# Performance work log

Hardware: AMD Instinct MI355X
Metric: run time of the kernel (lower is better)

## Reference

```python
import jax, jax.numpy as jnp
import numpy as np
from jax import lax

NUM_HEADS = 8
FACTOR = 2
DIM = 64


def _get_idx(h, w):
    # Frequency-magnitude reordering map from Attention.get_idx_map (static shapes).
    l2 = np.arange(w)[None, :]
    mu = np.arange(h // 2)[:, None] * l2                 # upper half outer product
    md = np.arange(h - h // 2)[::-1][:, None] * l2        # lower half, flipped rows
    m = np.concatenate([mu, md], 0).reshape(-1)
    idx = np.argsort(m, kind='stable')                    # gather permutation
    inv = np.argsort(idx)                                 # scatter (inverse) permutation
    return jnp.asarray(idx), jnp.asarray(inv)


def _dwconv3x3(x, w):
    # depthwise 3x3, stride 1, padding 1 (groups = channels)
    c = x.shape[1]
    return lax.conv_general_dilated(x, w[:, None, :, :], (1, 1), 'SAME',
                                    dimension_numbers=('NCHW', 'OIHW', 'NCHW'),
                                    feature_group_count=c)


def _fft_reorder(t, idx):
    # pad last dim to even, rfft2 (ortho), stack real/imag on channels, gather by idx
    b, c, h, w = t.shape
    pad_w = (-w) % 2
    t = jnp.pad(t, ((0, 0), (0, 0), (0, 0), (0, pad_w)))
    f = jnp.fft.rfft2(t, norm='ortho')                     # [b,c,h,w']
    r = jnp.concatenate([f.real, f.imag], axis=1)          # [b,2c,h,w']
    r = r.reshape(b, 2 * c, -1)[:, :, idx]                 # gather reorder
    return r, pad_w


def _softmax1(x):
    # non-standard softmax: exp(x) / (sum(exp(x)) + 1), no max-subtraction (faithful)
    e = jnp.exp(x)
    return e / (jnp.sum(e, axis=-1, keepdims=True) + 1.0)


def _l2norm(x):
    n = jnp.sqrt(jnp.sum(x * x, axis=-1, keepdims=True))
    return x / jnp.maximum(n, 1e-12)


def _split_heads(t):
    # 'b (head c) (factor hw) -> b head (c factor) hw'
    B, C2, Np = t.shape
    cc = C2 // NUM_HEADS
    t = t.reshape(B, NUM_HEADS, cc, FACTOR, Np // FACTOR)
    return t.reshape(B, NUM_HEADS, cc * FACTOR, Np // FACTOR)


def attention_forward(x, w_qkv, w_dw, w_proj, temperature):
    b, c, h, w = x.shape
    qkv = jnp.einsum('bchw,oc->bohw', x, w_qkv)            # 1x1 conv (3c out)
    qkv = _dwconv3x3(qkv, w_dw)
    q, k, v = jnp.split(qkv, 3, axis=1)

    wprime = (w + ((-w) % 2)) // 2 + 1                     # rfft last-dim size
    idx, inv = _get_idx(h, wprime)

    q, pad_w = _fft_reorder(q, idx)
    k, _ = _fft_reorder(k, idx)
    v, _ = _fft_reorder(v, idx)

    p = (-q.shape[-1]) % FACTOR                            # pad N to multiple of factor
    if p:
        pads = ((0, 0), (0, 0), (0, p))
        q, k, v = jnp.pad(q, pads), jnp.pad(k, pads), jnp.pad(v, pads)

    qh, kh, vh = _split_heads(q), _split_heads(k), _split_heads(v)
    qh, kh = _l2norm(qh), _l2norm(kh)

    attn = jnp.einsum('bhcn,bhdn->bhcd', qh, kh) * temperature[None]  # c x c, per head
    attn = _softmax1(attn)
    o = jnp.einsum('bhcd,bhdn->bhcn', attn, vh)

    # 'b head (c factor) hw -> b (head c) (factor hw)'
    B, H, CF, HW = o.shape
    o = o.reshape(B, H, CF // FACTOR, FACTOR, HW).reshape(B, H * (CF // FACTOR), FACTOR * HW)
    if p:
        o = o[:, :, :o.shape[-1] - p]
    o = o[:, :, inv]                                        # inverse permutation (scatter)
    o = o.reshape(B, 2 * c, h, wprime)
    oc = lax.complex(o[:, :c], o[:, c:])
    o = jnp.fft.irfft2(oc, norm='ortho')                    # [b,c,h,w+pad_w]
    if pad_w:
        o = o[:, :, :, :o.shape[-1] - pad_w]
    return jnp.einsum('bchw,oc->bohw', o, w_proj)           # project_out 1x1 conv


def setup_inputs() -> dict:
    key = jax.random.key(0)
    k1, k2, k3, k4 = jax.random.split(key, 4)
    b, c, h, w = 4, DIM, 256, 256
    return {
        'x': jax.random.normal(k1, (b, c, h, w), dtype=jnp.float32),
        'w_qkv': jax.random.normal(k2, (3 * c, c), dtype=jnp.float32) * 0.05,
        'w_dw': jax.random.normal(k3, (3 * c, 3, 3), dtype=jnp.float32) * 0.05,
        'w_proj': jax.random.normal(k4, (c, c), dtype=jnp.float32) * 0.05,
        'temperature': jnp.ones((NUM_HEADS, 1, 1), dtype=jnp.float32),
    }


def reference(x, w_qkv, w_dw, w_proj, temperature):
    return attention_forward(x, w_qkv, w_dw, w_proj, temperature)
```

## Files before the change

### kernel.cpp

```cpp
#include <hip/hip_runtime.h>
#include <math.h>

#define HW 65536
#define WP 129
#define NPOS 33024
#define NHALF 16512
#define MMAX 16257
#define PI_F 3.14159265358979f

__device__ __forceinline__ int rev7(int x){ return (int)(__brev((unsigned)x) >> 25); }
__device__ __forceinline__ int rev8(int x){ return (int)(__brev((unsigned)x) >> 24); }

__global__ void k_hist(int* __restrict__ hist) {
  int v = blockIdx.x*256 + threadIdx.x;
  if (v >= MMAX) return;
  int cnt;
  if (v == 0) cnt = 512;
  else {
    cnt = 0;
    for (int d = 1; d <= 127; ++d)
      if (v % d == 0 && v / d <= 128) cnt += 2;
  }
  hist[v] = cnt;
}

__global__ void k_scan(const int* __restrict__ hist, int* __restrict__ base) {
  __shared__ int part[512];
  int t = threadIdx.x;
  int lo = t*32, hi = lo+32; if (hi > MMAX) hi = MMAX;
  int s = 0;
  if (lo < MMAX) for (int i = lo; i < hi; ++i) s += hist[i];
  part[t] = s;
  __syncthreads();
  for (int off = 1; off < 512; off <<= 1) {
    int v = (t >= off) ? part[t-off] : 0;
    __syncthreads();
    part[t] += v;
    __syncthreads();
  }
  int acc = part[t] - s;
  if (lo < MMAX) for (int i = lo; i < hi; ++i) { base[i] = acc; acc += hist[i]; }
}

__global__ void k_build(const int* __restrict__ base, int* __restrict__ idx, int* __restrict__ inv) {
  int v = blockIdx.x*256 + threadIdx.x;
  if (v >= MMAX) return;
  int s = base[v];
  if (v == 0) {
    for (int j = 0; j < 129; ++j) { idx[s] = j; inv[j] = s; ++s; }
    for (int i = 1; i < 255; ++i) { int p = i*129; idx[s] = p; inv[p] = s; ++s; }
    for (int j = 0; j < 129; ++j) { int p = 255*129 + j; idx[s] = p; inv[p] = s; ++s; }
  } else {
    for (int i = 1; i < 255; ++i) {
      int d = (i < 128) ? i : 255 - i;
      if (v % d == 0) {
        int j = v / d;
        if (j <= 128) { int p = i*129 + j; idx[s] = p; inv[p] = s; ++s; }
      }
    }
  }
}

__global__ void k_maps(const int* __restrict__ idx, const int* __restrict__ inv,
                       int* __restrict__ partner_t, int* __restrict__ half_t) {
  int t = blockIdx.x*256 + threadIdx.x;
  if (t >= NPOS) return;
  int k = t >> 8, h = t & 255;
  int p = h*129 + k;
  int s = inv[p];
  int f = (s >= NHALF) ? 1 : 0;
  int s2 = f ? (s - NHALF) : (s + NHALF);
  int pp = idx[s2];
  int kk = pp % 129, hh = pp / 129;
  partner_t[t] = kk*256 + hh;
  half_t[t] = f;
}

__global__ void k_maps2(const int* __restrict__ idx,
                        int* __restrict__ t0n, int* __restrict__ t1n) {
  int n = blockIdx.x*256 + threadIdx.x;
  if (n >= NHALF) return;
  int p0 = idx[n], p1 = idx[n + NHALF];
  t0n[n] = (p0 % 129)*256 + p0/129;
  t1n[n] = (p1 % 129)*256 + p1/129;
}

__global__ void k_zero(float* __restrict__ g) {
  int i = blockIdx.x*256 + threadIdx.x;
  if (i < 34816) g[i] = 0.f;
}

__global__ __launch_bounds__(256) void k_conv64(const float* __restrict__ in,
        const float* __restrict__ w, float* __restrict__ outp) {
  __shared__ float wT[64][65];
  __shared__ float xs[16][260];
  int tid = threadIdx.x;
  int ti = tid >> 5, tj = tid & 31;
  int lb = blockIdx.y;
  int px0 = blockIdx.x * 256;
  const float* ib = in + (size_t)lb*64*HW + px0;
  for (int e = tid; e < 4096; e += 256) { int o = e >> 6, c = e & 63; wT[c][o] = w[e]; }
  float acc[64];
  #pragma unroll
  for (int z = 0; z < 64; ++z) acc[z] = 0.f;
  for (int cc = 0; cc < 4; ++cc) {
    __syncthreads();
    for (int e = tid; e < 1024; e += 256) {
      int c = e >> 6, p4 = (e & 63) << 2;
      *(float4*)&xs[c][p4] = *(const float4*)(ib + (size_t)(cc*16 + c)*HW + p4);
    }
    __syncthreads();
    #pragma unroll
    for (int k = 0; k < 16; ++k) {
      float wv[8], xv[8];
      *(float4*)&wv[0] = *(const float4*)&wT[cc*16+k][ti*8];
      *(float4*)&wv[4] = *(const float4*)&wT[cc*16+k][ti*8+4];
      *(float4*)&xv[0] = *(const float4*)&xs[k][tj*8];
      *(float4*)&xv[4] = *(const float4*)&xs[k][tj*8+4];
      #pragma unroll
      for (int o = 0; o < 8; ++o) {
        #pragma unroll
        for (int p = 0; p < 8; ++p)
          acc[o*8+p] += wv[o]*xv[p];
      }
    }
  }
  float* ob = outp + (size_t)lb*64*HW + px0 + tj*8;
  #pragma unroll
  for (int o = 0; o < 8; ++o) {
    *(float4*)(ob + (size_t)(ti*8+o)*HW)     = *(float4*)&acc[o*8];
    *(float4*)(ob + (size_t)(ti*8+o)*HW + 4) = *(float4*)&acc[o*8+4];
  }
}

__global__ __launch_bounds__(512) void k_dwrowfft(const float* __restrict__ tmp,
        const float* __restrict__ wdw, float* __restrict__ planes,
        int tensor, size_t psz) {
  __shared__ float rows[10][260];
  __shared__ float2 Z[8][128];
  __shared__ float2 X[8][132];
  int wave = threadIdx.x >> 6, lane = threadIdx.x & 63;
  int lb = blockIdx.z, c = blockIdx.y;
  int h0 = blockIdx.x * 8;
  const float* ib = tmp + ((size_t)lb*64 + c)*HW;
  for (int e = threadIdx.x; e < 2560; e += 512) {
    int r = e >> 8, col = e & 255;
    int y = h0 - 1 + r;
    rows[r][col] = (y >= 0 && y < 256) ? ib[y*256 + col] : 0.f;
  }
  const float* w9 = wdw + ((size_t)tensor*64 + c)*9;
  float w0=w9[0],w1=w9[1],w2=w9[2],w3=w9[3],w4=w9[4],w5=w9[5],w6=w9[6],w7=w9[7],w8=w9[8];
  __syncthreads();
  float d[4];
  #pragma unroll
  for (int q = 0; q < 4; ++q) {
    int col = (q < 2) ? (2*lane + q) : (128 + 2*lane + (q-2));
    float acc = rows[wave+0][col]*w1 + rows[wave+1][col]*w4 + rows[wave+2][col]*w7;
    if (col > 0)   acc += rows[wave+0][col-1]*w0 + rows[wave+1][col-1]*w3 + rows[wave+2][col-1]*w6;
    if (col < 255) acc += rows[wave+0][col+1]*w2 + rows[wave+1][col+1]*w5 + rows[wave+2][col+1]*w8;
    d[q] = acc;
  }
  Z[wave][rev7(lane)]    = make_float2(d[0], d[1]);
  Z[wave][rev7(lane+64)] = make_float2(d[2], d[3]);
  __syncthreads();
  for (int L = 1; L <= 64; L <<= 1) {
    int kk = lane & (L-1);
    int i0 = ((lane ^ kk) << 1) | kk;
    float sn, cs; sincosf(-PI_F * kk / L, &sn, &cs);
    float2 u = Z[wave][i0], t = Z[wave][i0+L];
    float tr = t.x*cs - t.y*sn;
    float ti = t.x*sn + t.y*cs;
    Z[wave][i0]   = make_float2(u.x+tr, u.y+ti);
    Z[wave][i0+L] = make_float2(u.x-tr, u.y-ti);
    __syncthreads();
  }
  for (int kk = lane; kk <= 128; kk += 64) {
    float2 Zk = Z[wave][kk & 127];
    float2 Zm = Z[wave][(128-kk) & 127];
    float Er = 0.5f*(Zk.x + Zm.x), Ei = 0.5f*(Zk.y - Zm.y);
    float Or = 0.5f*(Zk.y + Zm.y), Oi = 0.5f*(Zm.x - Zk.x);
    float sn, cs; sincosf(-PI_F * kk / 128.0f, &sn, &cs);
    float Xr = Er + cs*Or - sn*Oi;
    float Xi = Ei + cs*Oi + sn*Or;
    X[wave][kk] = make_float2(Xr*(1.0f/256.0f), Xi*(1.0f/256.0f));
  }
  __syncthreads();
  float* pre = planes + (size_t)(tensor*2)*psz + ((size_t)lb*64 + c)*NPOS;
  float* pim = pre + psz;
  for (int e = threadIdx.x; e < 1032; e += 512) {
    int k = e >> 3, hh = e & 7;
    float2 v = X[hh][k];
    pre[(size_t)k*256 + h0 + hh] = v.x;
    pim[(size_t)k*256 + h0 + hh] = v.y;
  }
}

__global__ __launch_bounds__(512) void k_colfft(float* __restrict__ planes,
        int tensor, size_t psz) {
  __shared__ float2 Z[8][258];
  int wave = threadIdx.x >> 6, lane = threadIdx.x & 63;
  int lb = blockIdx.z, c = blockIdx.y;
  int kreal = blockIdx.x*8 + wave;
  int k = (kreal < 129) ? kreal : 128;
  float* pre = planes + (size_t)(tensor*2)*psz + ((size_t)lb*64 + c)*NPOS + (size_t)k*256;
  float* pim = pre + psz;
  #pragma unroll
  for (int i = 0; i < 4; ++i) {
    int h = lane + 64*i;
    Z[wave][rev8(h)] = make_float2(pre[h], pim[h]);
  }
  __syncthreads();
  for (int L = 1; L <= 128; L <<= 1) {
    #pragma unroll
    for (int jj = 0; jj < 2; ++jj) {
      int j = lane + 64*jj;
      int kk = j & (L-1);
      int i0 = ((j ^ kk) << 1) | kk;
      float sn, cs; sincosf(-PI_F * kk / L, &sn, &cs);
      float2 u = Z[wave][i0], t = Z[wave][i0+L];
      float tr = t.x*cs - t.y*sn;
      float ti = t.x*sn + t.y*cs;
      Z[wave][i0]   = make_float2(u.x+tr, u.y+ti);
      Z[wave][i0+L] = make_float2(u.x-tr, u.y-ti);
    }
    __syncthreads();
  }
  if (kreal <= 128) {
    #pragma unroll
    for (int i = 0; i < 4; ++i) {
      float2 v = Z[wave][lane + 64*i];
      pre[lane+64*i] = v.x;
      pim[lane+64*i] = v.y;
    }
  }
}

__global__ __launch_bounds__(256) void k_t16(const float* __restrict__ P,
        float* __restrict__ T, const int* __restrict__ half_t,
        float* __restrict__ nq, float* __restrict__ nk, int b, size_t psz) {
  __shared__ float ld[256][18];
  int tn = blockIdx.y >> 3, h = blockIdx.y & 7;
  int t0 = blockIdx.x * 256;
  const float* src = P + (size_t)(tn*2 + (h>>2))*psz + ((size_t)(b*64 + (h&3)*16))*NPOS;
  int cr = threadIdx.x >> 4, ts = threadIdx.x & 15;
  float s0 = 0.f, s1 = 0.f;
  #pragma unroll
  for (int p2 = 0; p2 < 16; ++p2) {
    int tt = ts + p2*16;
    float v = src[(size_t)cr*NPOS + t0 + tt];
    ld[tt][cr] = v;
    if (tn < 2) { if (half_t[t0+tt]) s1 += v*v; else s0 += v*v; }
  }
  if (tn < 2) {
    s0 += __shfl_down(s0, 8, 16); s1 += __shfl_down(s1, 8, 16);
    s0 += __shfl_down(s0, 4, 16); s1 += __shfl_down(s1, 4, 16);
    s0 += __shfl_down(s0, 2, 16); s1 += __shfl_down(s1, 2, 16);
    s0 += __shfl_down(s0, 1, 16); s1 += __shfl_down(s1, 1, 16);
    if (ts == 0) {
      float* dn = (tn == 0) ? nq : nk;
      int bh = b*8 + h;
      atomicAdd(&dn[bh*32 + 2*cr],     s0);
      atomicAdd(&dn[bh*32 + 2*cr + 1], s1);
    }
  }
  __syncthreads();
  float* dst = T + ((size_t)blockIdx.y*NPOS + t0)*16;
  int cc = threadIdx.x & 15, tr = threadIdx.x >> 4;
  #pragma unroll
  for (int p2 = 0; p2 < 16; ++p2) {
    int tt = tr + p2*16;
    dst[(size_t)tt*16 + cc] = ld[tt][cc];
  }
}

__global__ __launch_bounds__(256) void k_gramn(const float* __restrict__ T,
        const int* __restrict__ t0n, const int* __restrict__ t1n,
        float* __restrict__ gram, int b) {
  __shared__ float q0s[16][68], q1s[16][68], k0s[16][68], k1s[16][68];
  __shared__ int tl[128];
  __shared__ float red[3][64][16];
  int tid = threadIdx.x;
  int np = tid >> 6, lane = tid & 63;
  int i = lane >> 3, j = lane & 7;
  int h = blockIdx.y;
  const float* Tq = T + (size_t)h*NPOS*16;
  const float* Tk = T + (size_t)(8 + h)*NPOS*16;
  float acc[16];
  #pragma unroll
  for (int z = 0; z < 16; ++z) acc[z] = 0.f;
  for (int it = 0; it < 3; ++it) {
    int n0 = (blockIdx.x*3 + it)*64;
    __syncthreads();
    if (tid < 128) tl[tid] = ((tid < 64) ? t0n[n0 + tid] : t1n[n0 + tid - 64]) * 16;
    __syncthreads();
    for (int e = tid; e < 1024; e += 256) {
      int nn = e >> 4, c2 = e & 15;
      int a0 = tl[nn], a1 = tl[64+nn];
      q0s[c2][nn] = Tq[(size_t)a0 + c2];
      q1s[c2][nn] = Tq[(size_t)a1 + c2];
      k0s[c2][nn] = Tk[(size_t)a0 + c2];
      k1s[c2][nn] = Tk[(size_t)a1 + c2];
    }
    __syncthreads();
    #pragma unroll
    for (int m = 0; m < 4; ++m) {
      int n = m*16 + np*4;
      float4 qA0 = *(const float4*)&q0s[i][n];
      float4 qB0 = *(const float4*)&q0s[i+8][n];
      float4 qA1 = *(const float4*)&q1s[i][n];
      float4 qB1 = *(const float4*)&q1s[i+8][n];
      float4 kA0 = *(const float4*)&k0s[j][n];
      float4 kB0 = *(const float4*)&k0s[j+8][n];
      float4 kA1 = *(const float4*)&k1s[j][n];
      float4 kB1 = *(const float4*)&k1s[j+8][n];
      const float* xa0 = (const float*)&qA0;
      const float* xa1 = (const float*)&qA1;
      const float* xb0 = (const float*)&qB0;
      const float* xb1 = (const float*)&qB1;
      const float* ya0 = (const float*)&kA0;
      const float* ya1 = (const float*)&kA1;
      const float* yb0 = (const float*)&kB0;
      const float* yb1 = (const float*)&kB1;
      #pragma unroll
      for (int nn = 0; nn < 4; ++nn) {
        float xA0 = xa0[nn], xA1 = xa1[nn], xB0 = xb0[nn], xB1 = xb1[nn];
        float yA0 = ya0[nn], yA1 = ya1[nn], yB0 = yb0[nn], yB1 = yb1[nn];
        acc[0]  += xA0*yA0; acc[1]  += xA0*yA1; acc[2]  += xA0*yB0; acc[3]  += xA0*yB1;
        acc[4]  += xA1*yA0; acc[5]  += xA1*yA1; acc[6]  += xA1*yB0; acc[7]  += xA1*yB1;
        acc[8]  += xB0*yA0; acc[9]  += xB0*yA1; acc[10] += xB0*yB0; acc[11] += xB0*yB1;
        acc[12] += xB1*yA0; acc[13] += xB1*yA1; acc[14] += xB1*yB0; acc[15] += xB1*yB1;
      }
    }
  }
  __syncthreads();
  if (np > 0) {
    #pragma unroll
    for (int z = 0; z < 16; ++z) red[np-1][lane][z] = acc[z];
  }
  __syncthreads();
  if (np == 0) {
    float* G = gram + (size_t)(b*8 + h)*1024;
    #pragma unroll
    for (int z = 0; z < 16; ++z) {
      float v = acc[z] + red[0][lane][z] + red[1][lane][z] + red[2][lane][z];
      int qs = z >> 2, ks = z & 3;
      int r  = 2*(i + 8*(qs>>1)) + (qs&1);
      int cl = 2*(j + 8*(ks>>1)) + (ks&1);
      atomicAdd(&G[r*32 + cl], v);
    }
  }
}

__global__ void k_attn(const float* __restrict__ gram, const float* __restrict__ nq,
                       const float* __restrict__ nk, const float* __restrict__ temp,
                       float* __restrict__ attn, int b0) {
  __shared__ float lnk[32];
  int bh = b0*8 + blockIdx.x, h = bh & 7;
  int r = threadIdx.x;
  if (r < 32) lnk[r] = fmaxf(sqrtf(nk[bh*32 + r]), 1e-12f);
  __syncthreads();
  if (r >= 32) return;
  float T = temp[h];
  float nqr = fmaxf(sqrtf(nq[bh*32 + r]), 1e-12f);
  float e[32]; float s = 0.f;
  #pragma unroll
  for (int c = 0; c < 32; ++c) {
    float g = gram[(size_t)bh*1024 + r*32 + c] / (nqr * lnk[c]) * T;
    e[c] = expf(g);
    s += e[c];
  }
  float is = 1.0f / (s + 1.0f);
  #pragma unroll
  for (int c = 0; c < 32; ++c) attn[(size_t)bh*1024 + r*32 + c] = e[c] * is;
}

__global__ __launch_bounds__(256) void k_on(const float* __restrict__ T,
    const float* __restrict__ attn, const int* __restrict__ partner_t,
    const int* __restrict__ half_t, float* __restrict__ O, int b, size_t psz) {
  __shared__ float At[1024];
  int hh = blockIdx.y;
  for (int e = threadIdx.x; e < 1024; e += 256)
    At[e] = attn[(size_t)(b*8 + hh)*1024 + e];
  __syncthreads();
  int t = blockIdx.x*256 + threadIdx.x;
  int f = half_t[t], pt = partner_t[t];
  const float* tv = T + (size_t)(16 + hh)*NPOS*16;
  const float4* va4 = (const float4*)(tv + (size_t)t*16);
  const float4* vb4 = (const float4*)(tv + (size_t)pt*16);
  float w0[16], w1[16];
  #pragma unroll
  for (int dq = 0; dq < 4; ++dq) {
    float4 a = va4[dq], bb = vb4[dq];
    w0[4*dq+0] = f ? bb.x : a.x;  w1[4*dq+0] = f ? a.x : bb.x;
    w0[4*dq+1] = f ? bb.y : a.y;  w1[4*dq+1] = f ? a.y : bb.y;
    w0[4*dq+2] = f ? bb.z : a.z;  w1[4*dq+2] = f ? a.z : bb.z;
    w0[4*dq+3] = f ? bb.w : a.w;  w1[4*dq+3] = f ? a.w : bb.w;
  }
  float* op = O + (size_t)(hh>=4 ? 1:0)*psz + ((size_t)(b*64 + (hh&3)*16))*NPOS;
  #pragma unroll
  for (int c = 0; c < 16; ++c) {
    const float4* Ar = (const float4*)&At[(2*c+f)*32];
    float acc = 0.f;
    #pragma unroll
    for (int d = 0; d < 8; ++d) {
      float4 a4 = Ar[d];
      acc += a4.x*w0[2*d] + a4.y*w1[2*d] + a4.z*w0[2*d+1] + a4.w*w1[2*d+1];
    }
    op[(size_t)c*NPOS + t] = acc;
  }
}

__global__ __launch_bounds__(256) void k_gram(const float* __restrict__ planes,
    const int* __restrict__ partner_t, const int* __restrict__ half_t,
    float* __restrict__ gram, float* __restrict__ nq, float* __restrict__ nk,
    int b0, size_t psz) {
  __shared__ float qa[16][65], ka[16][65], kb[16][65];
  __shared__ int ptn[64];
  __shared__ int hf[64];
  int lb = blockIdx.y >> 3, h = blockIdx.y & 7;
  int bh = (b0 + lb)*8 + h;
  const float* qp = planes + (size_t)(h>=4 ? 1:0)*psz + ((size_t)(lb*64 + (h&3)*16))*NPOS;
  const float* kp = planes + (size_t)(2 + (h>=4 ? 1:0))*psz + ((size_t)(lb*64 + (h&3)*16))*NPOS;
  int tc = threadIdx.x & 15, td = threadIdx.x >> 4;
  float a00=0.f,a01=0.f,a10=0.f,a11=0.f, q0=0.f,q1=0.f,k0a=0.f,k1a=0.f;
  for (int it = 0; it < 6; ++it) {
    int t0 = (blockIdx.x*6 + it)*64;
    if (threadIdx.x < 64) {
      ptn[threadIdx.x] = partner_t[t0 + threadIdx.x];
      hf[threadIdx.x]  = half_t[t0 + threadIdx.x];
    }
    __syncthreads();
    for (int e = threadIdx.x; e < 1024; e += 256) {
      int cc = e >> 6, j = e & 63;
      qa[cc][j] = qp[(size_t)cc*NPOS + t0 + j];
      ka[cc][j] = kp[(size_t)cc*NPOS + t0 + j];
      kb[cc][j] = kp[(size_t)cc*NPOS + ptn[j]];
    }
    __syncthreads();
    #pragma unroll 4
    for (int j = 0; j < 64; ++j) {
      float q = qa[tc][j], v1 = ka[td][j], v2 = kb[td][j];
      int f = hf[j];
      float p1 = q*v1, p2 = q*v2;
      if (f) { a11 += p1; a10 += p2; } else { a00 += p1; a01 += p2; }
      if (td == 0) { float qq = q*q; if (f) q1 += qq; else q0 += qq; }
      if (tc == 0) { float kk = v1*v1; if (f) k1a += kk; else k0a += kk; }
    }
    __syncthreads();
  }
  float* G = gram + (size_t)bh*1024;
  atomicAdd(&G[(2*tc+0)*32 + 2*td+0], a00);
  atomicAdd(&G[(2*tc+0)*32 + 2*td+1], a01);
  atomicAdd(&G[(2*tc+1)*32 + 2*td+0], a10);
  atomicAdd(&G[(2*tc+1)*32 + 2*td+1], a11);
  if (td == 0) { atomicAdd(&nq[bh*32 + 2*tc], q0); atomicAdd(&nq[bh*32 + 2*tc+1], q1); }
  if (tc == 0) { atomicAdd(&nk[bh*32 + 2*td], k0a); atomicAdd(&nk[bh*32 + 2*td+1], k1a); }
}

__global__ __launch_bounds__(256) void k_o(const float* __restrict__ planes,
    const float* __restrict__ attn, const int* __restrict__ partner_t,
    const int* __restrict__ half_t, float* __restrict__ O, int b0, size_t psz) {
  __shared__ float At[8][1024];
  int lb = blockIdx.y;
  for (int e = threadIdx.x; e < 8192; e += 256)
    At[e>>10][e&1023] = attn[((size_t)(b0+lb)*8)*1024 + e];
  __syncthreads();
  int t = blockIdx.x*256 + threadIdx.x;
  int f = half_t[t], pt = partner_t[t];
  #pragma unroll 1
  for (int hh = 0; hh < 8; ++hh) {
    const float* vp = planes + (size_t)(4 + (hh>=4 ? 1:0))*psz + ((size_t)(lb*64 + (hh&3)*16))*NPOS;
    float* op = O + (size_t)(hh>=4 ? 1:0)*psz + ((size_t)(lb*64 + (hh&3)*16))*NPOS;
    float w0[16], w1[16];
    #pragma unroll
    for (int d = 0; d < 16; ++d) {
      float va = vp[(size_t)d*NPOS + t];
      float vb = vp[(size_t)d*NPOS + pt];
      w0[d] = f ? vb : va;
      w1[d] = f ? va : vb;
    }
    #pragma unroll
    for (int c = 0; c < 16; ++c) {
      const float4* Ar = (const float4*)&At[hh][(2*c+f)*32];
      float acc = 0.f;
      #pragma unroll
      for (int d = 0; d < 8; ++d) {
        float4 a4 = Ar[d];
        acc += a4.x*w0[2*d] + a4.y*w1[2*d] + a4.z*w0[2*d+1] + a4.w*w1[2*d+1];
      }
      op[(size_t)c*NPOS + t] = acc;
    }
  }
}

__global__ __launch_bounds__(512) void k_colifft(const float* __restrict__ O,
        float2* __restrict__ IT, size_t psz) {
  __shared__ float2 Z[8][258];
  int wave = threadIdx.x >> 6, lane = threadIdx.x & 63;
  int lb = blockIdx.z, c = blockIdx.y;
  int kreal = blockIdx.x*8 + wave;
  int k = (kreal < 129) ? kreal : 128;
  const float* pre = O + ((size_t)lb*64 + c)*NPOS + (size_t)k*256;
  const float* pim = pre + psz;
  #pragma unroll
  for (int i = 0; i < 4; ++i) {
    int h = lane + 64*i;
    Z[wave][rev8(h)] = make_float2(pre[h], pim[h]);
  }
  __syncthreads();
  for (int L = 1; L <= 128; L <<= 1) {
    #pragma unroll
    for (int jj = 0; jj < 2; ++jj) {
      int j = lane + 64*jj;
      int kk = j & (L-1);
      int i0 = ((j ^ kk) << 1) | kk;
      float sn, cs; sincosf(PI_F * kk / L, &sn, &cs);
      float2 u = Z[wave][i0], t = Z[wave][i0+L];
      float tr = t.x*cs - t.y*sn;
      float ti = t.x*sn + t.y*cs;
      Z[wave][i0]   = make_float2(u.x+tr, u.y+ti);
      Z[wave][i0+L] = make_float2(u.x-tr, u.y-ti);
    }
    __syncthreads();
  }
  float2* outp = IT + ((size_t)lb*64 + c)*256*WP;
  int k0 = blockIdx.x*8;
  for (int e = threadIdx.x; e < 2048; e += 512) {
    int hpos = e >> 3, kk2 = e & 7;
    if (k0 + kk2 <= 128) {
      float2 v = Z[kk2][hpos];
      outp[(size_t)hpos*WP + k0 + kk2] = make_float2(v.x*(1.0f/256.0f), v.y*(1.0f/256.0f));
    }
  }
}

__global__ __launch_bounds__(512) void k_rowirfft(const float2* __restrict__ IT,
        float* __restrict__ sp) {
  __shared__ float2 Xl[8][132];
  __shared__ float2 Z[8][128];
  int wave = threadIdx.x >> 6, lane = threadIdx.x & 63;
  int lb = blockIdx.z, c = blockIdx.y;
  int h = blockIdx.x*8 + wave;
  const float2* row = IT + (((size_t)lb*64 + c)*256 + h)*WP;
  float2 v0 = row[lane];     if (lane == 0) v0.y = 0.f;
  float2 v1 = row[lane+64];
  Xl[wave][lane] = v0;
  Xl[wave][lane+64] = v1;
  if (lane == 0) { float2 vn = row[128]; vn.y = 0.f; Xl[wave][128] = vn; }
  __syncthreads();
  for (int u = 0; u < 2; ++u) {
    int kk = lane + 64*u;
    float2 Xk = Xl[wave][kk];
    float2 Xm = Xl[wave][128-kk];
    float Ar = Xk.x + Xm.x, Ai = Xk.y - Xm.y;
    float Br = Xk.x - Xm.x, Bi = Xk.y + Xm.y;
    float sn, cs; sincosf(PI_F * kk / 128.0f, &sn, &cs);
    float tr = cs*Br - sn*Bi, ti = cs*Bi + sn*Br;
    Z[wave][rev7(kk)] = make_float2(Ar - ti, Ai + tr);
  }
  __syncthreads();
  for (int L = 1; L <= 64; L <<= 1) {
    int kk = lane & (L-1);
    int i0 = ((lane ^ kk) << 1) | kk;
    float sn, cs; sincosf(PI_F * kk / L, &sn, &cs);
    float2 u2 = Z[wave][i0], t = Z[wave][i0+L];
    float tr = t.x*cs - t.y*sn;
    float ti = t.x*sn + t.y*cs;
    Z[wave][i0]   = make_float2(u2.x+tr, u2.y+ti);
    Z[wave][i0+L] = make_float2(u2.x-tr, u2.y-ti);
    __syncthreads();
  }
  float2* orow = (float2*)(sp + (((size_t)lb*64 + c)*256 + h)*256);
  orow[lane]    = Z[wave][lane];
  orow[lane+64] = Z[wave][lane+64];
}

extern "C" void kernel_launch(void* const* d_in, const int* in_sizes, int n_in,
                              void* d_out, int out_size, void* d_ws, size_t ws_size,
                              hipStream_t stream) {
  const float* x      = (const float*)d_in[0];
  const float* w_qkv  = (const float*)d_in[1];
  const float* w_dw   = (const float*)d_in[2];
  const float* w_proj = (const float*)d_in[3];
  const float* temp   = (const float*)d_in[4];
  float* out = (float*)d_out;

  char* ws = (char*)d_ws;
  int*   hist = (int*)(ws + 0);
  int*   base = (int*)(ws + 65536);
  int*   t0n  = (int*)(ws + 0);
  int*   t1n  = (int*)(ws + 66048);
  int*   idx  = (int*)(ws + 132352);
  int*   inv  = (int*)(ws + 264448);
  int*   ptn  = (int*)(ws + 396544);
  int*   hlf  = (int*)(ws + 528640);
  float* gram = (float*)(ws + 660736);
  float* nq   = (float*)(ws + 791808);
  float* nk   = (float*)(ws + 795904);
  float* attn = (float*)(ws + 800000);

  const size_t SMALL   = 1048576;
  const size_t PLANESB = 50724864;
  int NB = 1;
  if (ws_size >= SMALL + 2*PLANESB) NB = 2;
  if (ws_size >= SMALL + 4*PLANESB) NB = 4;

  float*  P   = (float*)(ws + SMALL);
  size_t  psz = (size_t)NB * 64 * NPOS;
  float*  O   = P;
  float2* IT  = (float2*)(P + 2*psz);
  float*  sp  = P + 4*psz;

  k_hist <<<dim3(64), dim3(256), 0, stream>>>(hist);
  k_scan <<<dim3(1),  dim3(512), 0, stream>>>(hist, base);
  k_build<<<dim3(64), dim3(256), 0, stream>>>(base, idx, inv);
  k_maps <<<dim3(129),dim3(256), 0, stream>>>(idx, inv, ptn, hlf);
  k_maps2<<<dim3(65), dim3(256), 0, stream>>>(idx, t0n, t1n);
  k_zero <<<dim3(136),dim3(256), 0, stream>>>(gram);

  if (NB == 4) {
    float* tmpb = out;
    for (int tn = 0; tn < 3; ++tn) {
      k_conv64  <<<dim3(256, 4), dim3(256), 0, stream>>>(x, w_qkv + (size_t)tn*64*64, tmpb);
      k_dwrowfft<<<dim3(32, 64, 4), dim3(512), 0, stream>>>(tmpb, w_dw, P, tn, psz);
      k_colfft  <<<dim3(17, 64, 4), dim3(512), 0, stream>>>(P, tn, psz);
    }
    float* T = out;
    for (int b = 0; b < 4; ++b) {
      k_t16  <<<dim3(129, 24), dim3(256), 0, stream>>>(P, T, hlf, nq, nk, b, psz);
      k_gramn<<<dim3(86, 8),   dim3(256), 0, stream>>>(T, t0n, t1n, gram, b);
      k_attn <<<dim3(8),       dim3(64),  0, stream>>>(gram, nq, nk, temp, attn, b);
      k_on   <<<dim3(129, 8),  dim3(256), 0, stream>>>(T, attn, ptn, hlf, O, b, psz);
    }
    k_colifft <<<dim3(17, 64, 4), dim3(512), 0, stream>>>(O, IT, psz);
    k_rowirfft<<<dim3(32, 64, 4), dim3(512), 0, stream>>>(IT, sp);
    k_conv64  <<<dim3(256, 4), dim3(256), 0, stream>>>(sp, w_proj, out);
  } else {
    for (int b0 = 0; b0 < 4; b0 += NB) {
      float* tmpb = out + (size_t)b0*64*HW;
      for (int tn = 0; tn < 3; ++tn) {
        k_conv64  <<<dim3(256, NB), dim3(256), 0, stream>>>(
            x + (size_t)b0*64*HW, w_qkv + (size_t)tn*64*64, tmpb);
        k_dwrowfft<<<dim3(32, 64, NB), dim3(512), 0, stream>>>(tmpb, w_dw, P, tn, psz);
        k_colfft  <<<dim3(17, 64, NB), dim3(512), 0, stream>>>(P, tn, psz);
      }
      k_gram<<<dim3(86, NB*8), dim3(256), 0, stream>>>(P, ptn, hlf, gram, nq, nk, b0, psz);
      k_attn<<<dim3(NB*8), dim3(64), 0, stream>>>(gram, nq, nk, temp, attn, b0);
      k_o   <<<dim3(129, NB), dim3(256), 0, stream>>>(P, attn, ptn, hlf, O, b0, psz);
      k_colifft <<<dim3(17, 64, NB), dim3(512), 0, stream>>>(O, IT, psz);
      k_rowirfft<<<dim3(32, 64, NB), dim3(512), 0, stream>>>(IT, sp);
      k_conv64  <<<dim3(256, NB), dim3(256), 0, stream>>>(sp, w_proj, out + (size_t)b0*64*HW);
    }
  }
}
```

Before: 1.153 ms.

## Use shared twiddle tables, split-complex LDS, and wave-local sync in FFT kernels

```diff
diff --git a/kernel.cpp b/kernel.cpp
--- a/kernel.cpp
+++ b/kernel.cpp
@@ -10,6 +10,10 @@
 
 __device__ __forceinline__ int rev7(int x){ return (int)(__brev((unsigned)x) >> 25); }
 __device__ __forceinline__ int rev8(int x){ return (int)(__brev((unsigned)x) >> 24); }
+
+__device__ __forceinline__ void wsync() {
+  asm volatile("s_waitcnt lgkmcnt(0)" ::: "memory");
+}
 
 __global__ void k_hist(int* __restrict__ hist) {
   int v = blockIdx.x*256 + threadIdx.x;
@@ -137,11 +141,16 @@
         const float* __restrict__ wdw, float* __restrict__ planes,
         int tensor, size_t psz) {
   __shared__ float rows[10][260];
-  __shared__ float2 Z[8][128];
-  __shared__ float2 X[8][132];
+  __shared__ float Zr[8][128], Zi[8][128];
+  __shared__ float Xr[8][132], Xi[8][132];
+  __shared__ float cs_t[132], sn_t[132];
   int wave = threadIdx.x >> 6, lane = threadIdx.x & 63;
   int lb = blockIdx.z, c = blockIdx.y;
   int h0 = blockIdx.x * 8;
+  if (threadIdx.x <= 128) {
+    float sn, cs; sincosf(-PI_F * threadIdx.x / 128.0f, &sn, &cs);
+    cs_t[threadIdx.x] = cs; sn_t[threadIdx.x] = sn;
+  }
   const float* ib = tmp + ((size_t)lb*64 + c)*HW;
   for (int e = threadIdx.x; e < 2560; e += 512) {
     int r = e >> 8, col = e & 255;
@@ -160,77 +169,90 @@
     if (col < 255) acc += rows[wave+0][col+1]*w2 + rows[wave+1][col+1]*w5 + rows[wave+2][col+1]*w8;
     d[q] = acc;
   }
-  Z[wave][rev7(lane)]    = make_float2(d[0], d[1]);
-  Z[wave][rev7(lane+64)] = make_float2(d[2], d[3]);
-  __syncthreads();
-  for (int L = 1; L <= 64; L <<= 1) {
+  int r0 = rev7(lane), r1 = rev7(lane+64);
+  Zr[wave][r0] = d[0]; Zi[wave][r0] = d[1];
+  Zr[wave][r1] = d[2]; Zi[wave][r1] = d[3];
+  wsync();
+  #pragma unroll
+  for (int s = 0; s < 7; ++s) {
+    int L = 1 << s;
     int kk = lane & (L-1);
     int i0 = ((lane ^ kk) << 1) | kk;
-    float sn, cs; sincosf(-PI_F * kk / L, &sn, &cs);
-    float2 u = Z[wave][i0], t = Z[wave][i0+L];
-    float tr = t.x*cs - t.y*sn;
-    float ti = t.x*sn + t.y*cs;
-    Z[wave][i0]   = make_float2(u.x+tr, u.y+ti);
-    Z[wave][i0+L] = make_float2(u.x-tr, u.y-ti);
-    __syncthreads();
+    int m = kk << (7 - s);
+    float cs = cs_t[m], sn = sn_t[m];
+    float ur = Zr[wave][i0],   ui = Zi[wave][i0];
+    float ar = Zr[wave][i0+L], ai = Zi[wave][i0+L];
+    float tr = ar*cs - ai*sn;
+    float ti = ar*sn + ai*cs;
+    Zr[wave][i0]   = ur+tr; Zi[wave][i0]   = ui+ti;
+    Zr[wave][i0+L] = ur-tr; Zi[wave][i0+L] = ui-ti;
+    wsync();
   }
   for (int kk = lane; kk <= 128; kk += 64) {
-    float2 Zk = Z[wave][kk & 127];
-    float2 Zm = Z[wave][(128-kk) & 127];
-    float Er = 0.5f*(Zk.x + Zm.x), Ei = 0.5f*(Zk.y - Zm.y);
-    float Or = 0.5f*(Zk.y + Zm.y), Oi = 0.5f*(Zm.x - Zk.x);
-    float sn, cs; sincosf(-PI_F * kk / 128.0f, &sn, &cs);
-    float Xr = Er + cs*Or - sn*Oi;
-    float Xi = Ei + cs*Oi + sn*Or;
-    X[wave][kk] = make_float2(Xr*(1.0f/256.0f), Xi*(1.0f/256.0f));
+    int a = kk & 127, bb = (128-kk) & 127;
+    float Zkr = Zr[wave][a],  Zki = Zi[wave][a];
+    float Zmr = Zr[wave][bb], Zmi = Zi[wave][bb];
+    float Er = 0.5f*(Zkr + Zmr), Ei = 0.5f*(Zki - Zmi);
+    float Or = 0.5f*(Zki + Zmi), Oi = 0.5f*(Zmr - Zkr);
+    float cs = cs_t[kk], sn = sn_t[kk];
+    Xr[wave][kk] = (Er + cs*Or - sn*Oi)*(1.0f/256.0f);
+    Xi[wave][kk] = (Ei + cs*Oi + sn*Or)*(1.0f/256.0f);
   }
   __syncthreads();
   float* pre = planes + (size_t)(tensor*2)*psz + ((size_t)lb*64 + c)*NPOS;
   float* pim = pre + psz;
   for (int e = threadIdx.x; e < 1032; e += 512) {
     int k = e >> 3, hh = e & 7;
-    float2 v = X[hh][k];
-    pre[(size_t)k*256 + h0 + hh] = v.x;
-    pim[(size_t)k*256 + h0 + hh] = v.y;
+    pre[(size_t)k*256 + h0 + hh] = Xr[hh][k];
+    pim[(size_t)k*256 + h0 + hh] = Xi[hh][k];
   }
 }
 
 __global__ __launch_bounds__(512) void k_colfft(float* __restrict__ planes,
         int tensor, size_t psz) {
-  __shared__ float2 Z[8][258];
+  __shared__ float Zr[8][256], Zi[8][256];
+  __shared__ float cs_t[132], sn_t[132];
   int wave = threadIdx.x >> 6, lane = threadIdx.x & 63;
   int lb = blockIdx.z, c = blockIdx.y;
   int kreal = blockIdx.x*8 + wave;
   int k = (kreal < 129) ? kreal : 128;
+  if (threadIdx.x < 128) {
+    float sn, cs; sincosf(-PI_F * threadIdx.x / 128.0f, &sn, &cs);
+    cs_t[threadIdx.x] = cs; sn_t[threadIdx.x] = sn;
+  }
   float* pre = planes + (size_t)(tensor*2)*psz + ((size_t)lb*64 + c)*NPOS + (size_t)k*256;
   float* pim = pre + psz;
   #pragma unroll
   for (int i = 0; i < 4; ++i) {
     int h = lane + 64*i;
-    Z[wave][rev8(h)] = make_float2(pre[h], pim[h]);
-  }
-  __syncthreads();
-  for (int L = 1; L <= 128; L <<= 1) {
+    int r = rev8(h);
+    Zr[wave][r] = pre[h]; Zi[wave][r] = pim[h];
+  }
+  __syncthreads();
+  #pragma unroll
+  for (int s = 0; s < 8; ++s) {
+    int L = 1 << s;
     #pragma unroll
     for (int jj = 0; jj < 2; ++jj) {
       int j = lane + 64*jj;
       int kk = j & (L-1);
       int i0 = ((j ^ kk) << 1) | kk;
-      float sn, cs; sincosf(-PI_F * kk / L, &sn, &cs);
-      float2 u = Z[wave][i0], t = Z[wave][i0+L];
-      float tr = t.x*cs - t.y*sn;
-      float ti = t.x*sn + t.y*cs;
-      Z[wave][i0]   = make_float2(u.x+tr, u.y+ti);
-      Z[wave][i0+L] = make_float2(u.x-tr, u.y-ti);
-    }
-    __syncthreads();
+      int m = kk << (7 - s);
+      float cs = cs_t[m], sn = sn_t[m];
+      float ur = Zr[wave][i0],   ui = Zi[wave][i0];
+      float ar = Zr[wave][i0+L], ai = Zi[wave][i0+L];
+      float tr = ar*cs - ai*sn;
+      float ti = ar*sn + ai*cs;
+      Zr[wave][i0]   = ur+tr; Zi[wave][i0]   = ui+ti;
+      Zr[wave][i0+L] = ur-tr; Zi[wave][i0+L] = ui-ti;
+    }
+    wsync();
   }
   if (kreal <= 128) {
     #pragma unroll
     for (int i = 0; i < 4; ++i) {
-      float2 v = Z[wave][lane + 64*i];
-      pre[lane+64*i] = v.x;
-      pim[lane+64*i] = v.y;
+      pre[lane+64*i] = Zr[wave][lane+64*i];
+      pim[lane+64*i] = Zi[wave][lane+64*i];
     }
   }
 }
@@ -495,41 +517,52 @@
 
 __global__ __launch_bounds__(512) void k_colifft(const float* __restrict__ O,
         float2* __restrict__ IT, size_t psz) {
-  __shared__ float2 Z[8][258];
+  __shared__ float Zr[8][256], Zi[8][256];
+  __shared__ float cs_t[132], sn_t[132];
   int wave = threadIdx.x >> 6, lane = threadIdx.x & 63;
   int lb = blockIdx.z, c = blockIdx.y;
   int kreal = blockIdx.x*8 + wave;
   int k = (kreal < 129) ? kreal : 128;
+  if (threadIdx.x < 128) {
+    float sn, cs; sincosf(PI_F * threadIdx.x / 128.0f, &sn, &cs);
+    cs_t[threadIdx.x] = cs; sn_t[threadIdx.x] = sn;
+  }
   const float* pre = O + ((size_t)lb*64 + c)*NPOS + (size_t)k*256;
   const float* pim = pre + psz;
   #pragma unroll
   for (int i = 0; i < 4; ++i) {
     int h = lane + 64*i;
-    Z[wave][rev8(h)] = make_float2(pre[h], pim[h]);
-  }
-  __syncthreads();
-  for (int L = 1; L <= 128; L <<= 1) {
+    int r = rev8(h);
+    Zr[wave][r] = pre[h]; Zi[wave][r] = pim[h];
+  }
+  __syncthreads();
+  #pragma unroll
+  for (int s = 0; s < 8; ++s) {
+    int L = 1 << s;
     #pragma unroll
     for (int jj = 0; jj < 2; ++jj) {
       int j = lane + 64*jj;
       int kk = j & (L-1);
       int i0 = ((j ^ kk) << 1) | kk;
-      float sn, cs; sincosf(PI_F * kk / L, &sn, &cs);
-      float2 u = Z[wave][i0], t = Z[wave][i0+L];
-      float tr = t.x*cs - t.y*sn;
-      float ti = t.x*sn + t.y*cs;
-      Z[wave][i0]   = make_float2(u.x+tr, u.y+ti);
-      Z[wave][i0+L] = make_float2(u.x-tr, u.y-ti);
-    }
-    __syncthreads();
-  }
+      int m = kk << (7 - s);
+      float cs = cs_t[m], sn = sn_t[m];
+      float ur = Zr[wave][i0],   ui = Zi[wave][i0];
+      float ar = Zr[wave][i0+L], ai = Zi[wave][i0+L];
+      float tr = ar*cs - ai*sn;
+      float ti = ar*sn + ai*cs;
+      Zr[wave][i0]   = ur+tr; Zi[wave][i0]   = ui+ti;
+      Zr[wave][i0+L] = ur-tr; Zi[wave][i0+L] = ui-ti;
+    }
+    wsync();
+  }
+  __syncthreads();
   float2* outp = IT + ((size_t)lb*64 + c)*256*WP;
   int k0 = blockIdx.x*8;
   for (int e = threadIdx.x; e < 2048; e += 512) {
     int hpos = e >> 3, kk2 = e & 7;
     if (k0 + kk2 <= 128) {
-      float2 v = Z[kk2][hpos];
-      outp[(size_t)hpos*WP + k0 + kk2] = make_float2(v.x*(1.0f/256.0f), v.y*(1.0f/256.0f));
+      outp[(size_t)hpos*WP + k0 + kk2] =
+        make_float2(Zr[kk2][hpos]*(1.0f/256.0f), Zi[kk2][hpos]*(1.0f/256.0f));
     }
   }
 }
@@ -537,10 +570,15 @@
 __global__ __launch_bounds__(512) void k_rowirfft(const float2* __restrict__ IT,
         float* __restrict__ sp) {
   __shared__ float2 Xl[8][132];
-  __shared__ float2 Z[8][128];
+  __shared__ float Zr[8][128], Zi[8][128];
+  __shared__ float cs_t[132], sn_t[132];
   int wave = threadIdx.x >> 6, lane = threadIdx.x & 63;
   int lb = blockIdx.z, c = blockIdx.y;
   int h = blockIdx.x*8 + wave;
+  if (threadIdx.x < 128) {
+    float sn, cs; sincosf(PI_F * threadIdx.x / 128.0f, &sn, &cs);
+    cs_t[threadIdx.x] = cs; sn_t[threadIdx.x] = sn;
+  }
   const float2* row = IT + (((size_t)lb*64 + c)*256 + h)*WP;
   float2 v0 = row[lane];     if (lane == 0) v0.y = 0.f;
   float2 v1 = row[lane+64];
@@ -548,31 +586,37 @@
   Xl[wave][lane+64] = v1;
   if (lane == 0) { float2 vn = row[128]; vn.y = 0.f; Xl[wave][128] = vn; }
   __syncthreads();
+  #pragma unroll
   for (int u = 0; u < 2; ++u) {
     int kk = lane + 64*u;
     float2 Xk = Xl[wave][kk];
     float2 Xm = Xl[wave][128-kk];
     float Ar = Xk.x + Xm.x, Ai = Xk.y - Xm.y;
     float Br = Xk.x - Xm.x, Bi = Xk.y + Xm.y;
-    float sn, cs; sincosf(PI_F * kk / 128.0f, &sn, &cs);
+    float cs = cs_t[kk], sn = sn_t[kk];
     float tr = cs*Br - sn*Bi, ti = cs*Bi + sn*Br;
-    Z[wave][rev7(kk)] = make_float2(Ar - ti, Ai + tr);
-  }
-  __syncthreads();
-  for (int L = 1; L <= 64; L <<= 1) {
+    int r = rev7(kk);
+    Zr[wave][r] = Ar - ti; Zi[wave][r] = Ai + tr;
+  }
+  wsync();
+  #pragma unroll
+  for (int s = 0; s < 7; ++s) {
+    int L = 1 << s;
     int kk = lane & (L-1);
     int i0 = ((lane ^ kk) << 1) | kk;
-    float sn, cs; sincosf(PI_F * kk / L, &sn, &cs);
-    float2 u2 = Z[wave][i0], t = Z[wave][i0+L];
-    float tr = t.x*cs - t.y*sn;
-    float ti = t.x*sn + t.y*cs;
-    Z[wave][i0]   = make_float2(u2.x+tr, u2.y+ti);
-    Z[wave][i0+L] = make_float2(u2.x-tr, u2.y-ti);
-    __syncthreads();
+    int m = kk << (7 - s);
+    float cs = cs_t[m], sn = sn_t[m];
+    float ur = Zr[wave][i0],   ui = Zi[wave][i0];
+    float ar = Zr[wave][i0+L], ai = Zi[wave][i0+L];
+    float tr = ar*cs - ai*sn;
+    float ti = ar*sn + ai*cs;
+    Zr[wave][i0]   = ur+tr; Zi[wave][i0]   = ui+ti;
+    Zr[wave][i0+L] = ur-tr; Zi[wave][i0+L] = ui-ti;
+    wsync();
   }
   float2* orow = (float2*)(sp + (((size_t)lb*64 + c)*256 + h)*256);
-  orow[lane]    = Z[wave][lane];
-  orow[lane+64] = Z[wave][lane+64];
+  orow[lane]    = make_float2(Zr[wave][lane],    Zi[wave][lane]);
+  orow[lane+64] = make_float2(Zr[wave][lane+64], Zi[wave][lane+64]);
 }
 
 extern "C" void kernel_launch(void* const* d_in, const int* in_sizes, int n_in,
```

New measurement: 1.061 ms. 1.09x faster.
